# Optimization experiments

Measured on AMD Instinct MI355X. Metric: run time of the kernel, lower is better.

The kernel has to match this reference:

```python
import jax, jax.numpy as jnp
import numpy as np

DELTA_V = 0.5
DELTA_D = 1.5
ALPHA = 1.0
BETA = 1.0
GAMMA = 0.001
K = 64  # max number of instance ids per batch element


def _safe_sqrt(sq):
    # sqrt with zero-safe gradient: exact where sq > 0, returns 0 otherwise
    pos = sq > 0
    return jnp.sqrt(jnp.where(pos, sq, 1.0)) * pos.astype(sq.dtype)


def setup_inputs() -> dict:
    key = jax.random.key(0)
    k1, k2 = jax.random.split(key)
    B, N, D = 16, 65536, 32
    embeddings = jax.random.normal(k1, (B, N, D), dtype=jnp.float32)
    instance_ids = jax.random.randint(k2, (B, N), 0, K, dtype=jnp.int32)
    mask = jnp.ones((B, N), dtype=bool)
    return {"embeddings": embeddings, "instance_ids": instance_ids, "mask": mask}


def reference(embeddings, instance_ids, mask):
    B, N, D = embeddings.shape
    f32 = embeddings.dtype
    valid = mask & (instance_ids >= 0)
    # flat segment id per point; invalid points go to dump segment B*K
    batch_off = jnp.arange(B, dtype=jnp.int32)[:, None] * K
    seg = jnp.where(valid, batch_off + instance_ids, B * K).reshape(-1)
    w = valid.reshape(-1).astype(f32)
    flat = embeddings.reshape(-1, D)

    # per-instance sums / counts -> means  (segment reduce, memory-bound)
    sums = jax.ops.segment_sum(flat * w[:, None], seg, num_segments=B * K + 1)[: B * K]
    counts = jax.ops.segment_sum(w, seg, num_segments=B * K + 1)[: B * K]
    means_flat = sums / jnp.maximum(counts, 1.0)[:, None]  # (B*K, D)
    present = (counts > 0).reshape(B, K)                   # (B, K)
    num_inst = present.sum(-1).astype(f32)                 # (B,)
    valid_b = (num_inst >= 2).astype(f32)                  # batches counted as samples

    # ---- variance (pull) loss ----
    seg_clip = jnp.minimum(seg, B * K - 1)
    diff = flat - means_flat[seg_clip]                     # (B*N, D)
    dist = _safe_sqrt((diff * diff).sum(-1))
    pen = jnp.maximum(dist - DELTA_V, 0.0) ** 2 * w
    inst_pen = jax.ops.segment_sum(pen, seg, num_segments=B * K + 1)[: B * K]
    inst_pen = (inst_pen / jnp.maximum(counts, 1.0)).reshape(B, K)
    var_b = (inst_pen * present).sum(-1) / jnp.maximum(num_inst, 1.0)

    # ---- distance (push) loss: pairwise over instance means ----
    means = means_flat.reshape(B, K, D)
    dsq = ((means[:, :, None, :] - means[:, None, :, :]) ** 2).sum(-1)  # (B, K, K)
    iu = jnp.arange(K)
    pair_m = present[:, :, None] & present[:, None, :] & (iu[:, None] < iu[None, :])
    pair_mf = pair_m.astype(f32)
    pdist = _safe_sqrt(jnp.where(pair_m, dsq, 1.0)) * pair_mf
    pen2 = jnp.maximum(2.0 * DELTA_D - pdist, 0.0) ** 2 * pair_mf
    num_pairs = num_inst * (num_inst - 1.0) / 2.0
    dist_b = pen2.sum((1, 2)) / jnp.maximum(num_pairs, 1.0)

    # ---- regularization loss ----
    mnorm = _safe_sqrt((means * means).sum(-1)) * present.astype(f32)  # (B, K)
    reg_b = mnorm.sum(-1) / jnp.maximum(num_inst, 1.0)

    denom = jnp.maximum(valid_b.sum(), 1.0)
    var_loss = (var_b * valid_b).sum() / denom
    dist_loss = (dist_b * valid_b).sum() / denom
    reg_loss = (reg_b * valid_b).sum() / denom
    total = ALPHA * var_loss + BETA * dist_loss + GAMMA * reg_loss
    return jnp.stack([total, var_loss, dist_loss, reg_loss])
```

## Files before the change

### kernel.cpp

```cpp
#include <hip/hip_runtime.h>
#include <cstdint>

#define BB 16
#define NN 65536
#define DD 32
#define KK 64
#define DELTA_V 0.5f
#define DELTA_D 1.5f

typedef short bf16x8 __attribute__((ext_vector_type(8)));
typedef float f32x16 __attribute__((ext_vector_type(16)));

__device__ __forceinline__ short f2bf(float x) {
    union { float f; unsigned u; } v; v.f = x;
    const unsigned r = v.u + 0x7FFFu + ((v.u >> 16) & 1u);
    return (short)(r >> 16);
}

#define K1_BPB 64
#define K1_PPB 1024

__global__ __launch_bounds__(256, 4) void k_accum(
    const float* __restrict__ emb, const int* __restrict__ ids,
    const int* __restrict__ mask, float* __restrict__ parts,
    float* __restrict__ pcnt)
{
    __shared__ float tbl[4][64][32];
    __shared__ float lc2[4][64];
    const int tid  = threadIdx.x;
    const int w    = tid >> 6, lane = tid & 63;
    const int half = lane >> 5, d32 = lane & 31;
    const int b    = blockIdx.x >> 6;
    const int blk  = blockIdx.x & 63;
    const size_t pw = (size_t)b * NN + (size_t)blk * K1_PPB + (size_t)w * 256;

    f32x16 acc0 = {}, acc1 = {};
    int c0 = 0, c1 = 0;
    const int m0 = d32, m1 = d32 + 32;

    const int* idsb = ids + pw;
    const int* mskb = mask + pw;
    const float* eb = emb + (pw + (size_t)half * 8) * DD + d32;

    float xa[32], xb[32];
    int idr, mkr;
#pragma unroll
    for (int j = 0; j < 32; ++j)
        xa[j] = eb[(size_t)(((j >> 3) * 16) + (j & 7)) * DD];
    idr = idsb[lane]; mkr = mskb[lane];

#pragma unroll
    for (int s = 0; s < 4; ++s) {
        int idr2 = 0, mkr2 = 0;
        if (s < 3) {
            const float* eb2 = eb + (size_t)(s + 1) * 64 * DD;
#pragma unroll
            for (int j = 0; j < 32; ++j)
                xb[j] = eb2[(size_t)(((j >> 3) * 16) + (j & 7)) * DD];
            idr2 = idsb[(s + 1) * 64 + lane];
            mkr2 = mskb[(s + 1) * 64 + lane];
        }
        const int vid = (mkr != 0 && (unsigned)idr < KK) ? idr : -1;
#pragma unroll
        for (int q = 0; q < 4; ++q) {
            bf16x8 bfB, a0, a1;
#pragma unroll
            for (int e = 0; e < 8; ++e) {
                bfB[e] = f2bf(xa[q * 8 + e]);
                const int s_lo = __builtin_amdgcn_readlane(vid, q * 16 + e);
                const int s_hi = __builtin_amdgcn_readlane(vid, q * 16 + 8 + e);
                const int sel  = half ? s_hi : s_lo;
                const bool h0 = (sel == m0), h1 = (sel == m1);
                a0[e] = h0 ? (short)0x3F80 : (short)0;
                a1[e] = h1 ? (short)0x3F80 : (short)0;
                c0 += h0 ? 1 : 0;
                c1 += h1 ? 1 : 0;
            }
            acc0 = __builtin_amdgcn_mfma_f32_32x32x16_bf16(a0, bfB, acc0, 0, 0, 0);
            acc1 = __builtin_amdgcn_mfma_f32_32x32x16_bf16(a1, bfB, acc1, 0, 0, 0);
        }
        if (s < 3) {
#pragma unroll
            for (int j = 0; j < 32; ++j) xa[j] = xb[j];
            idr = idr2; mkr = mkr2;
        }
    }

#pragma unroll
    for (int r = 0; r < 16; ++r) {
        const int mrow = (r & 3) + 8 * (r >> 2) + 4 * half;
        tbl[w][mrow][d32]      = acc0[r];
        tbl[w][32 + mrow][d32] = acc1[r];
    }
    c0 += __shfl_down(c0, 32);
    c1 += __shfl_down(c1, 32);
    if (lane < 32) { lc2[w][lane] = (float)c0; lc2[w][lane + 32] = (float)c1; }
    __syncthreads();

    float* pb = parts + (size_t)blockIdx.x * 2048;
    for (int i = tid; i < 2048; i += 256) {
        const int row = i >> 5, col = i & 31;
        pb[i] = tbl[0][row][col] + tbl[1][row][col]
              + tbl[2][row][col] + tbl[3][row][col];
    }
    if (tid < KK)
        pcnt[(size_t)blockIdx.x * KK + tid] =
            lc2[0][tid] + lc2[1][tid] + lc2[2][tid] + lc2[3][tid];
}

__global__ __launch_bounds__(256) void k_reduce_push(
    const float* __restrict__ parts, const float* __restrict__ pcnt,
    float* __restrict__ mu, float* __restrict__ regb,
    float* __restrict__ distb)
{
    const int b = blockIdx.x;
    const int tid = threadIdx.x;
    __shared__ float lm[KK][DD + 1];
    __shared__ float lcnt[KK];
    __shared__ float red[4];

    if (tid < KK) {
        float s = 0.f;
        for (int j = 0; j < K1_BPB; ++j)
            s += pcnt[((size_t)b * K1_BPB + j) * KK + tid];
        lcnt[tid] = s;
        mu[(size_t)b * KK * 36 + tid * 36 + 32] = s;
        mu[(size_t)b * KK * 36 + tid * 36 + 33] = 1.f / fmaxf(s, 1.f);
    }
    __syncthreads();

    for (int e = tid; e < KK * DD; e += 256) {
        float s = 0.f;
        for (int j = 0; j < K1_BPB; ++j)
            s += parts[((size_t)b * K1_BPB + j) * (KK * DD) + e];
        const int k = e >> 5, d = e & 31;
        const float m = s / fmaxf(lcnt[k], 1.f);
        lm[k][d] = m;
        mu[(size_t)b * KK * 36 + k * 36 + d] = m;
    }
    __syncthreads();

    float ninst = 0.f;
    if (tid < KK) {
        const float c = lcnt[tid];
        const float pres = (c > 0.f) ? 1.f : 0.f;
        float sq = 0.f;
#pragma unroll
        for (int d = 0; d < DD; ++d) { const float m = lm[tid][d]; sq = fmaf(m, m, sq); }
        float nm = ((sq > 0.f) ? sqrtf(sq) : 0.f) * pres;
        float pn = pres;
        for (int off = 32; off; off >>= 1) {
            pn += __shfl_down(pn, off);
            nm += __shfl_down(nm, off);
        }
        if (tid == 0) {
            ninst = pn;
            regb[b] = nm / fmaxf(pn, 1.f);
        }
    }

    float acc = 0.f;
    for (int idx = tid; idx < KK * KK; idx += 256) {
        const int i = idx >> 6, j = idx & 63;
        if (i < j && lcnt[i] > 0.f && lcnt[j] > 0.f) {
            float dsq = 0.f;
#pragma unroll
            for (int d = 0; d < DD; ++d) {
                const float df = lm[i][d] - lm[j][d];
                dsq = fmaf(df, df, dsq);
            }
            const float pd = (dsq > 0.f) ? sqrtf(dsq) : 0.f;
            const float pen = fmaxf(2.f * DELTA_D - pd, 0.f);
            acc = fmaf(pen, pen, acc);
        }
    }
    for (int off = 32; off; off >>= 1) acc += __shfl_down(acc, off);
    if ((tid & 63) == 0) red[tid >> 6] = acc;
    __syncthreads();
    if (tid == 0) {
        const float tot = red[0] + red[1] + red[2] + red[3];
        const float np = ninst * (ninst - 1.f) * 0.5f;
        distb[b] = tot / fmaxf(np, 1.f);
    }
}

#define K2_BPB 64
#define K2_PTS 1024

__global__ __launch_bounds__(256) void k_pull(
    const float* __restrict__ emb, const int* __restrict__ ids,
    const int* __restrict__ mask, const float* __restrict__ mu,
    float* __restrict__ varpart)
{
    __shared__ float smu[KK][36];
    __shared__ float red[4];
    const int tid = threadIdx.x;
    const int w = tid >> 6, lane = tid & 63;
    const int pl = lane >> 3;
    const int pc = lane & 7;
    const int b   = blockIdx.x >> 6;
    const int blk = blockIdx.x & 63;

    const float* mub = mu + (size_t)b * KK * 36;
    for (int i = tid; i < KK * 36; i += 256) ((float*)smu)[i] = mub[i];
    __syncthreads();

    const size_t p0 = (size_t)b * NN + (size_t)blk * K2_PTS + (size_t)w * 256;
    float accv = 0.f;
    for (int t = 0; t < 4; ++t) {
        const size_t pt0 = p0 + t * 64;
        const int idr = ids[pt0 + lane];
        const int mkr = mask[pt0 + lane];
        const int vid = (mkr != 0 && (unsigned)idr < KK) ? idr : -1;
        const float4* ep4 = (const float4*)(emb + pt0 * DD);
#pragma unroll
        for (int g = 0; g < 8; ++g) {
            const float4 x = ep4[g * 64 + lane];
            const int sid = __shfl(vid, g * 8 + pl);
            const int row = (sid >= 0) ? sid : 0;
            const float4 m4 = *(const float4*)&smu[row][4 * pc];
            float a = x.x - m4.x; float dsq = a * a;
            a = x.y - m4.y; dsq = fmaf(a, a, dsq);
            a = x.z - m4.z; dsq = fmaf(a, a, dsq);
            a = x.w - m4.w; dsq = fmaf(a, a, dsq);
            dsq += __shfl_xor(dsq, 1);
            dsq += __shfl_xor(dsq, 2);
            dsq += __shfl_xor(dsq, 4);
            if (pc == 0 && sid >= 0) {
                const float dist = (dsq > 0.f) ? sqrtf(dsq) : 0.f;
                float pen = fmaxf(dist - DELTA_V, 0.f);
                accv = fmaf(pen * pen, smu[row][33], accv);
            }
        }
    }
    for (int off = 32; off; off >>= 1) accv += __shfl_down(accv, off);
    if (lane == 0) red[w] = accv;
    __syncthreads();
    if (tid == 0)
        varpart[blockIdx.x] = red[0] + red[1] + red[2] + red[3];
}

__global__ __launch_bounds__(64) void k_final(
    const float* __restrict__ mu, const float* __restrict__ varpart,
    const float* __restrict__ regb, const float* __restrict__ distb,
    float* __restrict__ out)
{
    const int tid = threadIdx.x;
    __shared__ float s_var[BB], s_valid[BB];
    if (tid < BB) {
        const int b = tid;
        float ni = 0.f;
        for (int k = 0; k < KK; ++k)
            ni += (mu[(size_t)b * KK * 36 + k * 36 + 32] > 0.f) ? 1.f : 0.f;
        float vs = 0.f;
        for (int j = 0; j < K2_BPB; ++j) vs += varpart[b * K2_BPB + j];
        s_var[tid]   = vs / fmaxf(ni, 1.f);
        s_valid[tid] = (ni >= 2.f) ? 1.f : 0.f;
    }
    __syncthreads();
    if (tid == 0) {
        float denom = 0.f, v = 0.f, d = 0.f, r = 0.f;
        for (int b = 0; b < BB; ++b) {
            const float vb = s_valid[b];
            denom += vb;
            v += s_var[b] * vb;
            d += distb[b] * vb;
            r += regb[b] * vb;
        }
        denom = fmaxf(denom, 1.f);
        v /= denom; d /= denom; r /= denom;
        out[0] = v + d + 0.001f * r;
        out[1] = v;
        out[2] = d;
        out[3] = r;
    }
}

extern "C" void kernel_launch(void* const* d_in, const int* in_sizes, int n_in,
                              void* d_out, int out_size, void* d_ws, size_t ws_size,
                              hipStream_t stream)
{
    const float* emb  = (const float*)d_in[0];
    const int*   ids  = (const int*)d_in[1];
    const int*   mask = (const int*)d_in[2];

    float* ws      = (float*)d_ws;
    float* parts   = ws;
    float* pcnt    = parts + (size_t)BB * K1_BPB * KK * DD;
    float* mu      = pcnt + (size_t)BB * K1_BPB * KK;
    float* varpart = mu + (size_t)BB * KK * 36;
    float* regb    = varpart + BB * K2_BPB;
    float* distb   = regb + BB;

    k_accum<<<BB * K1_BPB, 256, 0, stream>>>(emb, ids, mask, parts, pcnt);
    k_reduce_push<<<BB, 256, 0, stream>>>(parts, pcnt, mu, regb, distb);
    k_pull<<<BB * K2_BPB, 256, 0, stream>>>(emb, ids, mask, mu, varpart);
    k_final<<<1, 64, 0, stream>>>(mu, varpart, regb, distb, (float*)d_out);
}
```

Before: 92.41 us.

## Stage embeddings via global_load_lds double buffering instead of register prefetch

Replaces the per-lane strided register loads of embeddings with direct global-to-LDS 16-byte async copies into a per-wave double buffer, using waitcnt to overlap the next 32-point chunk's load with the current chunk's MFMA work. The ids and mask are now read as one int4 per lane up front, and instance ids are fetched with readlane from the packed vector. This cuts register pressure and makes global loads fully coalesced, at the cost of extra LDS reads and reuse of the staging buffer as the reduction table. It relies on correct vmcnt accounting, and there is no wave-level LDS barrier after the async copies.

```diff
diff --git a/kernel.cpp b/kernel.cpp
--- a/kernel.cpp
+++ b/kernel.cpp
@@ -17,6 +17,12 @@
     return (short)(r >> 16);
 }
 
+__device__ __forceinline__ void gll16(const float* g, float* l) {
+    __builtin_amdgcn_global_load_lds(
+        (const __attribute__((address_space(1))) unsigned int*)g,
+        (__attribute__((address_space(3))) unsigned int*)l, 16, 0, 0);
+}
+
 #define K1_BPB 64
 #define K1_PPB 1024
 
@@ -25,7 +31,7 @@
     const int* __restrict__ mask, float* __restrict__ parts,
     float* __restrict__ pcnt)
 {
-    __shared__ float tbl[4][64][32];
+    __shared__ float stage[4][2][32][32];
     __shared__ float lc2[4][64];
     const int tid  = threadIdx.x;
     const int w    = tid >> 6, lane = tid & 63;
@@ -38,37 +44,46 @@
     int c0 = 0, c1 = 0;
     const int m0 = d32, m1 = d32 + 32;
 
-    const int* idsb = ids + pw;
-    const int* mskb = mask + pw;
-    const float* eb = emb + (pw + (size_t)half * 8) * DD + d32;
-
-    float xa[32], xb[32];
-    int idr, mkr;
-#pragma unroll
-    for (int j = 0; j < 32; ++j)
-        xa[j] = eb[(size_t)(((j >> 3) * 16) + (j & 7)) * DD];
-    idr = idsb[lane]; mkr = mskb[lane];
-
-#pragma unroll
-    for (int s = 0; s < 4; ++s) {
-        int idr2 = 0, mkr2 = 0;
-        if (s < 3) {
-            const float* eb2 = eb + (size_t)(s + 1) * 64 * DD;
-#pragma unroll
-            for (int j = 0; j < 32; ++j)
-                xb[j] = eb2[(size_t)(((j >> 3) * 16) + (j & 7)) * DD];
-            idr2 = idsb[(s + 1) * 64 + lane];
-            mkr2 = mskb[(s + 1) * 64 + lane];
-        }
-        const int vid = (mkr != 0 && (unsigned)idr < KK) ? idr : -1;
-#pragma unroll
-        for (int q = 0; q < 4; ++q) {
+    const int4 idv4 = *(const int4*)(ids + pw + lane * 4);
+    const int4 mkv4 = *(const int4*)(mask + pw + lane * 4);
+    int v4[4];
+    v4[0] = (mkv4.x != 0 && (unsigned)idv4.x < KK) ? idv4.x : -1;
+    v4[1] = (mkv4.y != 0 && (unsigned)idv4.y < KK) ? idv4.y : -1;
+    v4[2] = (mkv4.z != 0 && (unsigned)idv4.z < KK) ? idv4.z : -1;
+    v4[3] = (mkv4.w != 0 && (unsigned)idv4.w < KK) ? idv4.w : -1;
+
+    const float* ebase = emb + pw * DD;
+    float* buf0 = &stage[w][0][0][0];
+    float* buf1 = &stage[w][1][0][0];
+
+#pragma unroll
+    for (int i = 0; i < 4; ++i)
+        gll16(ebase + i * 256 + lane * 4, buf0 + i * 256);
+
+#pragma unroll
+    for (int s = 0; s < 8; ++s) {
+        float* cur = (s & 1) ? buf1 : buf0;
+        float* nxt = (s & 1) ? buf0 : buf1;
+        if (s < 7) {
+            const float* gs = ebase + (size_t)(s + 1) * 1024;
+#pragma unroll
+            for (int i = 0; i < 4; ++i)
+                gll16(gs + i * 256 + lane * 4, nxt + i * 256);
+            asm volatile("s_waitcnt vmcnt(4)" ::: "memory");
+        } else {
+            asm volatile("s_waitcnt vmcnt(0)" ::: "memory");
+        }
+        __builtin_amdgcn_sched_barrier(0);
+
+#pragma unroll
+        for (int g = 0; g < 2; ++g) {
             bf16x8 bfB, a0, a1;
 #pragma unroll
             for (int e = 0; e < 8; ++e) {
-                bfB[e] = f2bf(xa[q * 8 + e]);
-                const int s_lo = __builtin_amdgcn_readlane(vid, q * 16 + e);
-                const int s_hi = __builtin_amdgcn_readlane(vid, q * 16 + 8 + e);
+                bfB[e] = f2bf(cur[(g * 16 + half * 8 + e) * 32 + d32]);
+                const int pe = s * 32 + g * 16 + e;
+                const int s_lo = __builtin_amdgcn_readlane(v4[e & 3], pe >> 2);
+                const int s_hi = __builtin_amdgcn_readlane(v4[e & 3], (pe + 8) >> 2);
                 const int sel  = half ? s_hi : s_lo;
                 const bool h0 = (sel == m0), h1 = (sel == m1);
                 a0[e] = h0 ? (short)0x3F80 : (short)0;
@@ -79,13 +94,10 @@
             acc0 = __builtin_amdgcn_mfma_f32_32x32x16_bf16(a0, bfB, acc0, 0, 0, 0);
             acc1 = __builtin_amdgcn_mfma_f32_32x32x16_bf16(a1, bfB, acc1, 0, 0, 0);
         }
-        if (s < 3) {
-#pragma unroll
-            for (int j = 0; j < 32; ++j) xa[j] = xb[j];
-            idr = idr2; mkr = mkr2;
-        }
-    }
-
+    }
+    __syncthreads();
+
+    float (*tbl)[64][32] = (float(*)[64][32])&stage[0][0][0][0];
 #pragma unroll
     for (int r = 0; r < 16; ++r) {
         const int mrow = (r & 3) + 8 * (r >> 2) + 4 * half;
```

New measurement: 93.46 us. No clear change (+1.1%).

## Parallelize mean reduction, move push loss into pull, fuse final via atomic

Applied to the files above, without the earlier changes.

The 16-block reduce-and-push kernel becomes a 256-block kernel that only reduces partial sums and counts into means. The pairwise push and regularization terms now run in the first pull block of each batch. The final reduction is folded into the pull kernel through a last-block atomic counter, which removes one launch. The accum kernel's launch-bound occupancy hint is also lowered from 4 to 2. The pull blocks that do the push work take longer, and correctness now depends on the atomic counter and its memory ordering.

```diff
diff --git a/kernel.cpp b/kernel.cpp
--- a/kernel.cpp
+++ b/kernel.cpp
@@ -20,7 +20,7 @@
 #define K1_BPB 64
 #define K1_PPB 1024
 
-__global__ __launch_bounds__(256, 4) void k_accum(
+__global__ __launch_bounds__(256, 2) void k_accum(
     const float* __restrict__ emb, const int* __restrict__ ids,
     const int* __restrict__ mask, float* __restrict__ parts,
     float* __restrict__ pcnt)
@@ -108,92 +108,58 @@
             lc2[0][tid] + lc2[1][tid] + lc2[2][tid] + lc2[3][tid];
 }
 
-__global__ __launch_bounds__(256) void k_reduce_push(
+__global__ __launch_bounds__(256) void k_mid(
     const float* __restrict__ parts, const float* __restrict__ pcnt,
-    float* __restrict__ mu, float* __restrict__ regb,
-    float* __restrict__ distb)
+    float* __restrict__ mu, int* bar)
 {
-    const int b = blockIdx.x;
+    const int gb  = blockIdx.x;
+    const int b   = gb >> 4, seg = gb & 15;
     const int tid = threadIdx.x;
-    __shared__ float lm[KK][DD + 1];
-    __shared__ float lcnt[KK];
-    __shared__ float red[4];
-
-    if (tid < KK) {
-        float s = 0.f;
-        for (int j = 0; j < K1_BPB; ++j)
-            s += pcnt[((size_t)b * K1_BPB + j) * KK + tid];
-        lcnt[tid] = s;
-        mu[(size_t)b * KK * 36 + tid * 36 + 32] = s;
-        mu[(size_t)b * KK * 36 + tid * 36 + 33] = 1.f / fmaxf(s, 1.f);
-    }
-    __syncthreads();
-
-    for (int e = tid; e < KK * DD; e += 256) {
-        float s = 0.f;
-        for (int j = 0; j < K1_BPB; ++j)
-            s += parts[((size_t)b * K1_BPB + j) * (KK * DD) + e];
-        const int k = e >> 5, d = e & 31;
-        const float m = s / fmaxf(lcnt[k], 1.f);
-        lm[k][d] = m;
-        mu[(size_t)b * KK * 36 + k * 36 + d] = m;
-    }
-    __syncthreads();
-
-    float ninst = 0.f;
-    if (tid < KK) {
-        const float c = lcnt[tid];
-        const float pres = (c > 0.f) ? 1.f : 0.f;
-        float sq = 0.f;
-#pragma unroll
-        for (int d = 0; d < DD; ++d) { const float m = lm[tid][d]; sq = fmaf(m, m, sq); }
-        float nm = ((sq > 0.f) ? sqrtf(sq) : 0.f) * pres;
-        float pn = pres;
-        for (int off = 32; off; off >>= 1) {
-            pn += __shfl_down(pn, off);
-            nm += __shfl_down(nm, off);
-        }
-        if (tid == 0) {
-            ninst = pn;
-            regb[b] = nm / fmaxf(pn, 1.f);
-        }
-    }
-
-    float acc = 0.f;
-    for (int idx = tid; idx < KK * KK; idx += 256) {
-        const int i = idx >> 6, j = idx & 63;
-        if (i < j && lcnt[i] > 0.f && lcnt[j] > 0.f) {
-            float dsq = 0.f;
-#pragma unroll
-            for (int d = 0; d < DD; ++d) {
-                const float df = lm[i][d] - lm[j][d];
-                dsq = fmaf(df, df, dsq);
-            }
-            const float pd = (dsq > 0.f) ? sqrtf(dsq) : 0.f;
-            const float pen = fmaxf(2.f * DELTA_D - pd, 0.f);
-            acc = fmaf(pen, pen, acc);
-        }
-    }
-    for (int off = 32; off; off >>= 1) acc += __shfl_down(acc, off);
-    if ((tid & 63) == 0) red[tid >> 6] = acc;
-    __syncthreads();
-    if (tid == 0) {
-        const float tot = red[0] + red[1] + red[2] + red[3];
-        const float np = ninst * (ninst - 1.f) * 0.5f;
-        distb[b] = tot / fmaxf(np, 1.f);
+    __shared__ float red2[2][128];
+    __shared__ float rc4[4];
+    if (gb == 0 && tid == 0) bar[0] = 0;
+
+    const int k0 = seg * 4;
+    {
+        const int w = tid >> 6, lane = tid & 63;
+        float cv = pcnt[((size_t)(b * K1_BPB + lane)) * KK + k0 + w];
+        for (int off = 32; off; off >>= 1) cv += __shfl_down(cv, off);
+        if (lane == 0) {
+            mu[((size_t)b * KK + k0 + w) * 36 + 32] = cv;
+            const float rc = 1.f / fmaxf(cv, 1.f);
+            mu[((size_t)b * KK + k0 + w) * 36 + 33] = rc;
+            rc4[w] = rc;
+        }
+    }
+    const int e  = seg * 128 + (tid & 127);
+    const int jh = tid >> 7;
+    float s = 0.f;
+    const float* pp = parts + ((size_t)(b * K1_BPB + jh * 32)) * 2048 + e;
+#pragma unroll 4
+    for (int j = 0; j < 32; ++j) s += pp[(size_t)j * 2048];
+    red2[jh][tid & 127] = s;
+    __syncthreads();
+    if (tid < 128) {
+        const int k = e >> 5;
+        mu[((size_t)b * KK + k) * 36 + (e & 31)] =
+            (red2[0][tid] + red2[1][tid]) * rc4[k - k0];
     }
 }
 
 #define K2_BPB 64
 #define K2_PTS 1024
-
-__global__ __launch_bounds__(256) void k_pull(
+#define GRID3 (BB * K2_BPB)
+
+__global__ __launch_bounds__(256) void k_pull_final(
     const float* __restrict__ emb, const int* __restrict__ ids,
     const int* __restrict__ mask, const float* __restrict__ mu,
-    float* __restrict__ varpart)
+    float* varpart, float* aux, int* bar, float* __restrict__ out)
 {
     __shared__ float smu[KK][36];
     __shared__ float red[4];
+    __shared__ float part[256];
+    __shared__ float sf[4][BB];
+    __shared__ int s_last;
     const int tid = threadIdx.x;
     const int w = tid >> 6, lane = tid & 63;
     const int pl = lane >> 3;
@@ -204,6 +170,53 @@
     const float* mub = mu + (size_t)b * KK * 36;
     for (int i = tid; i < KK * 36; i += 256) ((float*)smu)[i] = mub[i];
     __syncthreads();
+
+    if (blk == 0) {
+        float ninst = 0.f;
+        if (tid < KK) {
+            const float c = smu[tid][32];
+            const float pres = (c > 0.f) ? 1.f : 0.f;
+            float sq = 0.f;
+#pragma unroll
+            for (int d = 0; d < DD; ++d) { const float m = smu[tid][d]; sq = fmaf(m, m, sq); }
+            float nm = ((sq > 0.f) ? sqrtf(sq) : 0.f) * pres;
+            float pn = pres;
+            for (int off = 32; off; off >>= 1) {
+                pn += __shfl_down(pn, off);
+                nm += __shfl_down(nm, off);
+            }
+            if (tid == 0) {
+                ninst = pn;
+                aux[b]      = nm / fmaxf(pn, 1.f);
+                aux[32 + b] = pn;
+            }
+        }
+        float acc = 0.f;
+        for (int idx = tid; idx < KK * KK; idx += 256) {
+            const int i = idx >> 6, j = idx & 63;
+            if (i < j && smu[i][32] > 0.f && smu[j][32] > 0.f) {
+                float dsq = 0.f;
+#pragma unroll
+                for (int d = 0; d < DD; ++d) {
+                    const float df = smu[i][d] - smu[j][d];
+                    dsq = fmaf(df, df, dsq);
+                }
+                const float pd = (dsq > 0.f) ? sqrtf(dsq) : 0.f;
+                const float pen = fmaxf(2.f * DELTA_D - pd, 0.f);
+                acc = fmaf(pen, pen, acc);
+            }
+        }
+        for (int off = 32; off; off >>= 1) acc += __shfl_down(acc, off);
+        if ((tid & 63) == 0) red[tid >> 6] = acc;
+        __syncthreads();
+        if (tid == 0) {
+            const float tot = red[0] + red[1] + red[2] + red[3];
+            const float ni = aux[32 + b];
+            const float np = ni * (ni - 1.f) * 0.5f;
+            aux[16 + b] = tot / fmaxf(np, 1.f);
+        }
+        __syncthreads();
+    }
 
     const size_t p0 = (size_t)b * NN + (size_t)blk * K2_PTS + (size_t)w * 256;
     float accv = 0.f;
@@ -238,41 +251,49 @@
     __syncthreads();
     if (tid == 0)
         varpart[blockIdx.x] = red[0] + red[1] + red[2] + red[3];
-}
-
-__global__ __launch_bounds__(64) void k_final(
-    const float* __restrict__ mu, const float* __restrict__ varpart,
-    const float* __restrict__ regb, const float* __restrict__ distb,
-    float* __restrict__ out)
-{
-    const int tid = threadIdx.x;
-    __shared__ float s_var[BB], s_valid[BB];
-    if (tid < BB) {
-        const int b = tid;
-        float ni = 0.f;
-        for (int k = 0; k < KK; ++k)
-            ni += (mu[(size_t)b * KK * 36 + k * 36 + 32] > 0.f) ? 1.f : 0.f;
-        float vs = 0.f;
-        for (int j = 0; j < K2_BPB; ++j) vs += varpart[b * K2_BPB + j];
-        s_var[tid]   = vs / fmaxf(ni, 1.f);
-        s_valid[tid] = (ni >= 2.f) ? 1.f : 0.f;
-    }
-    __syncthreads();
+
     if (tid == 0) {
-        float denom = 0.f, v = 0.f, d = 0.f, r = 0.f;
-        for (int b = 0; b < BB; ++b) {
-            const float vb = s_valid[b];
-            denom += vb;
-            v += s_var[b] * vb;
-            d += distb[b] * vb;
-            r += regb[b] * vb;
-        }
-        denom = fmaxf(denom, 1.f);
-        v /= denom; d /= denom; r /= denom;
-        out[0] = v + d + 0.001f * r;
-        out[1] = v;
-        out[2] = d;
-        out[3] = r;
+        const int ret = __hip_atomic_fetch_add(bar, 1, __ATOMIC_RELEASE,
+                                               __HIP_MEMORY_SCOPE_AGENT);
+        s_last = (ret == GRID3 - 1) ? 1 : 0;
+        if (s_last)
+            (void)__hip_atomic_load(bar, __ATOMIC_ACQUIRE,
+                                    __HIP_MEMORY_SCOPE_AGENT);
+    }
+    __syncthreads();
+    if (s_last) {
+        {
+            const float4 v4 = ((const float4*)varpart)[tid];
+            part[tid] = v4.x + v4.y + v4.z + v4.w;
+        }
+        __syncthreads();
+        if (tid < BB) {
+            float vs = 0.f;
+#pragma unroll
+            for (int j = 0; j < 16; ++j) vs += part[tid * 16 + j];
+            const float ni = aux[32 + tid];
+            sf[0][tid] = vs / fmaxf(ni, 1.f);
+            sf[1][tid] = (ni >= 2.f) ? 1.f : 0.f;
+            sf[2][tid] = aux[tid];
+            sf[3][tid] = aux[16 + tid];
+        }
+        __syncthreads();
+        if (tid == 0) {
+            float denom = 0.f, v = 0.f, d = 0.f, r = 0.f;
+            for (int bb = 0; bb < BB; ++bb) {
+                const float vb = sf[1][bb];
+                denom += vb;
+                v += sf[0][bb] * vb;
+                d += sf[3][bb] * vb;
+                r += sf[2][bb] * vb;
+            }
+            denom = fmaxf(denom, 1.f);
+            v /= denom; d /= denom; r /= denom;
+            out[0] = v + d + 0.001f * r;
+            out[1] = v;
+            out[2] = d;
+            out[3] = r;
+        }
     }
 }
 
@@ -289,11 +310,11 @@
     float* pcnt    = parts + (size_t)BB * K1_BPB * KK * DD;
     float* mu      = pcnt + (size_t)BB * K1_BPB * KK;
     float* varpart = mu + (size_t)BB * KK * 36;
-    float* regb    = varpart + BB * K2_BPB;
-    float* distb   = regb + BB;
+    float* aux     = varpart + GRID3;
+    int*   bar     = (int*)(aux + 64);
 
     k_accum<<<BB * K1_BPB, 256, 0, stream>>>(emb, ids, mask, parts, pcnt);
-    k_reduce_push<<<BB, 256, 0, stream>>>(parts, pcnt, mu, regb, distb);
-    k_pull<<<BB * K2_BPB, 256, 0, stream>>>(emb, ids, mask, mu, varpart);
-    k_final<<<1, 64, 0, stream>>>(mu, varpart, regb, distb, (float*)d_out);
-}
+    k_mid<<<256, 256, 0, stream>>>(parts, pcnt, mu, bar);
+    k_pull_final<<<GRID3, 256, 0, stream>>>(emb, ids, mask, mu, varpart,
+                                            aux, bar, (float*)d_out);
+}
```

Result: faster. 87.67 us (-5.1%).
